# Kernel tuning notes

Hardware: AMD Instinct MI355X
Metric: run time of the kernel (lower is better)

Reference implementation:

```python
import jax, jax.numpy as jnp
import numpy as np

NVAR, B, C, H, W = 3, 4, 256, 64, 64
C1 = C // 2          # dat channels (nc)
C2 = C - C1
HEADS = 4
HC = C1 // HEADS     # head channels
STRIDE = 4
KS = 4
HK, WK = H // STRIDE, W // STRIDE
NS = HK * WK         # n_sample
RPE_H, RPE_W = 2 * H - 1, 2 * W - 1
NPAIR = 3


def _grid_sample(img, grid):
    # img [B,C,Hi,Wi]; grid [B,Hg,Wg,2] = (x,y) in [-1,1]; bilinear, align_corners=True, zero-pad
    Bn, Cn, Hi, Wi = img.shape
    x = (grid[..., 0] + 1.0) * 0.5 * (Wi - 1)
    y = (grid[..., 1] + 1.0) * 0.5 * (Hi - 1)
    x0 = jnp.floor(x)
    y0 = jnp.floor(y)
    wx = x - x0
    wy = y - y0
    x0i = x0.astype(jnp.int32)
    y0i = y0.astype(jnp.int32)
    imt = img.transpose(0, 2, 3, 1)  # [B,Hi,Wi,C]
    bidx = jnp.arange(Bn)[:, None, None]

    def corner(yi, xi, wgt):
        ok = ((xi >= 0) & (xi < Wi) & (yi >= 0) & (yi < Hi)).astype(img.dtype)
        val = imt[bidx, jnp.clip(yi, 0, Hi - 1), jnp.clip(xi, 0, Wi - 1)]  # [B,Hg,Wg,C]
        return val * (wgt * ok)[..., None]

    out = (corner(y0i, x0i, (1 - wx) * (1 - wy))
           + corner(y0i, x0i + 1, wx * (1 - wy))
           + corner(y0i + 1, x0i, (1 - wx) * wy)
           + corner(y0i + 1, x0i + 1, wx * wy))
    return out.transpose(0, 3, 1, 2)  # [B,C,Hg,Wg]


def _ref_points(hk, wk):
    # normalized sampling-grid reference points, (y,x) order
    ry = (jnp.linspace(0.5, hk - 0.5, hk) / (hk - 1.0)) * 2.0 - 1.0
    rx = (jnp.linspace(0.5, wk - 0.5, wk) / (wk - 1.0)) * 2.0 - 1.0
    return jnp.stack(jnp.meshgrid(ry, rx, indexing='ij'), axis=-1)  # [hk,wk,2]


def _q_grid(h, w):
    gy = (jnp.arange(h, dtype=jnp.float32) / (h - 1.0)) * 2.0 - 1.0
    gx = (jnp.arange(w, dtype=jnp.float32) / (w - 1.0)) * 2.0 - 1.0
    return jnp.stack(jnp.meshgrid(gy, gx, indexing='ij'), axis=-1).reshape(h * w, 2)


def _conv1x1(x, w, b=None):
    y = jnp.einsum('oc,bchw->bohw', w, x)
    return y if b is None else y + b[None, :, None, None]


def _dat_block(q_in, kv_in, pWq, pbq, pWk, pbk, pWv, pbv, pWo, pbo,
               pdw_w, pdw_b, pln_g, pln_b, ppw_w, prpe):
    Bn = q_in.shape[0]
    q = _conv1x1(q_in, pWq, pbq)  # [B,C1,H,W]
    # offset net: depthwise 4x4 stride-4 conv -> channel LN -> GELU -> 1x1 conv to 2
    off = jax.lax.conv_general_dilated(
        q, pdw_w, (STRIDE, STRIDE), 'VALID',
        dimension_numbers=('NCHW', 'OIHW', 'NCHW'),
        feature_group_count=C1) + pdw_b[None, :, None, None]  # [B,C1,HK,WK]
    mu = off.mean(axis=1, keepdims=True)
    var = ((off - mu) ** 2).mean(axis=1, keepdims=True)
    off = (off - mu) * jax.lax.rsqrt(var + 1e-5) * pln_g[None, :, None, None] + pln_b[None, :, None, None]
    off = jax.nn.gelu(off, approximate=False)
    offset = _conv1x1(off, ppw_w).transpose(0, 2, 3, 1)  # [B,HK,WK,2] (dy,dx)
    # offset_range_factor = -1 -> no tanh scaling, clamp pos into [-1,1]
    pos = jnp.clip(offset + _ref_points(HK, WK)[None], -1.0, 1.0)  # [B,HK,WK,2]
    xs = _grid_sample(kv_in, pos[..., ::-1])  # sample kv at deformed points -> [B,C1,HK,WK]
    k = _conv1x1(xs, pWk, pbk).reshape(Bn, HEADS, HC, NS)
    v = _conv1x1(xs, pWv, pbv).reshape(Bn, HEADS, HC, NS)
    qh = q.reshape(Bn, HEADS, HC, H * W)
    attn = jnp.einsum('bhcm,bhcn->bhmn', qh, k) * (HC ** -0.5)  # [B,h,HW,NS]
    # relative position bias sampled from rpe table
    disp = (_q_grid(H, W)[None, :, None, :] - pos.reshape(Bn, 1, NS, 2)) * 0.5  # [B,HW,NS,2]
    rpe_b = jnp.broadcast_to(prpe[None], (Bn, HEADS, RPE_H, RPE_W))
    bias = _grid_sample(rpe_b, disp[..., ::-1])  # [B,h,HW,NS]
    attn = jax.nn.softmax(attn + bias, axis=-1)
    out = jnp.einsum('bhmn,bhcn->bhcm', attn, v).reshape(Bn, C1, H, W)
    return _conv1x1(out, pWo, pbo)


def _forward(xs, params):
    results = []
    num = 0
    for i in range(NVAR):
        res = xs[i]
        for j in range(i):
            attn_out = _dat_block(xs[i][:, :C1], xs[j][:, :C1],
                                  *(p[num] for p in params))
            # torch: res -= -cat(zeros[:,:C2], attn)  => add attn on channels C2:
            res = res.at[:, C2:].add(attn_out)
            num += 1
        results.append(res)
    return jnp.stack(results)  # [NVAR,B,C,H,W]


def setup_inputs() -> dict:
    key = jax.random.key(0)
    ks = jax.random.split(key, 4)
    d = {}
    for n, k in zip(['x0', 'x1', 'x2'], jax.random.split(ks[0], 3)):
        d[n] = jax.random.normal(k, (B, C, H, W), jnp.float32)

    def w(k, shape, s=0.02):
        return jax.random.normal(k, shape, jnp.float32) * s

    kk = jax.random.split(ks[1], 8)
    d['Wq'] = w(kk[0], (NPAIR, C1, C1))
    d['bq'] = jnp.zeros((NPAIR, C1), jnp.float32)
    d['Wk'] = w(kk[1], (NPAIR, C1, C1))
    d['bk'] = jnp.zeros((NPAIR, C1), jnp.float32)
    d['Wv'] = w(kk[2], (NPAIR, C1, C1))
    d['bv'] = jnp.zeros((NPAIR, C1), jnp.float32)
    d['Wo'] = w(kk[3], (NPAIR, C1, C1))
    d['bo'] = jnp.zeros((NPAIR, C1), jnp.float32)
    d['dw_w'] = w(kk[4], (NPAIR, C1, 1, KS, KS), 0.1)
    d['dw_b'] = jnp.zeros((NPAIR, C1), jnp.float32)
    d['ln_g'] = jnp.ones((NPAIR, C1), jnp.float32)
    d['ln_b'] = jnp.zeros((NPAIR, C1), jnp.float32)
    d['pw_w'] = w(kk[5], (NPAIR, 2, C1), 0.1)
    d['rpe'] = w(kk[6], (NPAIR, HEADS, RPE_H, RPE_W), 0.01)
    return d


def reference(x0, x1, x2, Wq, bq, Wk, bk, Wv, bv, Wo, bo,
              dw_w, dw_b, ln_g, ln_b, pw_w, rpe):
    params = (Wq, bq, Wk, bk, Wv, bv, Wo, bo, dw_w, dw_b, ln_g, ln_b, pw_w, rpe)
    out = _forward([x0, x1, x2], params)
    flow = jnp.zeros((NVAR, x0.shape[0]), out.dtype)
    return out, flow
```

## Files before the change

kernel.cpp:

```cpp
#include <hip/hip_runtime.h>
#include <math.h>

#define NVAR 3
#define BB 4
#define CC 256
#define C1 128
#define HEADS 4
#define HH 64
#define WW 64
#define HW 4096
#define RPE_W 127
#define NP 3
#define SCALE 0.17677669529663687f

typedef short bf16x8 __attribute__((ext_vector_type(8)));
typedef float f32x4 __attribute__((ext_vector_type(4)));

__device__ __forceinline__ unsigned short f2bf(float f) {
    unsigned int u = __float_as_uint(f);
    u += 0x7fffu + ((u >> 16) & 1u);
    return (unsigned short)(u >> 16);
}
__device__ __forceinline__ float bflo(unsigned u) { return __uint_as_float(u << 16); }
__device__ __forceinline__ float bfhi(unsigned u) { return __uint_as_float(u & 0xffff0000u); }

__global__ __launch_bounds__(256) void copy_init(const float* __restrict__ x0,
                                                 float* __restrict__ out) {
    const long long n4 = (long long)BB * CC * HW / 4;
    long long stride = (long long)gridDim.x * blockDim.x;
    for (long long i = (long long)blockIdx.x * blockDim.x + threadIdx.x;
         i < n4 + 12; i += stride) {
        if (i < n4) ((float4*)out)[i] = ((const float4*)x0)[i];
        else out[3LL * BB * CC * HW + (i - n4)] = 0.f;
    }
}

__global__ __launch_bounds__(256) void prep_const(const float* __restrict__ rpe,
                                                  const float* __restrict__ Wq,
                                                  const float* __restrict__ Wo,
                                                  const float* __restrict__ Wk,
                                                  const float* __restrict__ Wv,
                                                  unsigned short* __restrict__ tabbf,
                                                  unsigned short* __restrict__ wqh,
                                                  unsigned short* __restrict__ wql,
                                                  unsigned short* __restrict__ woh,
                                                  unsigned short* __restrict__ wkh,
                                                  unsigned short* __restrict__ wvh) {
    int blk = blockIdx.x;
    if (blk < 12) {
        const float* src = rpe + (long long)blk * RPE_W * RPE_W;
        unsigned short* dst = tabbf + (long long)blk * 16384;
        for (int idx = threadIdx.x; idx < 16384; idx += 256) {
            int y = idx >> 7, x = idx & 127;
            float v = (y < RPE_W && x < RPE_W) ? src[y * RPE_W + x] : 0.f;
            dst[idx] = f2bf(v);
        }
    } else if (blk < 15) {
        int p = blk - 12;
        for (int i = threadIdx.x; i < 16384; i += 256) {
            float w = Wq[p * 16384 + i];
            unsigned short h = f2bf(w);
            wqh[p * 16384 + i] = h;
            wql[p * 16384 + i] = f2bf(w - bflo((unsigned)h));
        }
    } else if (blk < 18) {
        int p = blk - 15;
        for (int i = threadIdx.x; i < 16384; i += 256)
            woh[p * 16384 + i] = f2bf(Wo[p * 16384 + i]);
    } else if (blk < 21) {
        int p = blk - 18;
        for (int i = threadIdx.x; i < 16384; i += 256)
            wkh[p * 16384 + i] = f2bf(Wk[p * 16384 + i]);
    } else {
        int p = blk - 21;
        for (int i = threadIdx.x; i < 16384; i += 256)
            wvh[p * 16384 + i] = f2bf(Wv[p * 16384 + i]);
    }
}

__global__ __launch_bounds__(256) void conv_q(const float* __restrict__ x1,
                                              const float* __restrict__ x2,
                                              const unsigned short* __restrict__ wqh,
                                              const unsigned short* __restrict__ wql,
                                              const float* __restrict__ bq,
                                              float* __restrict__ qbuf,
                                              unsigned short* __restrict__ qbf,
                                              float* __restrict__ out) {
    int wid = threadIdx.x >> 6, lane = threadIdx.x & 63;
    int g = lane >> 4, lm = lane & 15;
    int gw = blockIdx.x * 4 + wid;
    int mt = gw & 255;
    int pb = gw >> 8;
    int p = pb >> 2, b = pb & 3;
    const float* X = ((p == 0) ? x1 : x2) + (long long)b * CC * HW;
    int m = mt * 16 + lm;
    float* outc = (p < 2)
        ? out + (((long long)((p + 1) * 4 + b)) * CC) * HW + m
        : nullptr;

    bf16x8 bhi[4], blo[4];
#pragma unroll
    for (int ksl = 0; ksl < 4; ksl++) {
        float v[8];
#pragma unroll
        for (int j = 0; j < 8; j++) {
            int k = ksl * 32 + 8 * g + j;
            v[j] = X[(long long)k * HW + m];
            if (outc) outc[(long long)k * HW] = v[j];
        }
        union { unsigned u[4]; bf16x8 v; } H, L;
#pragma unroll
        for (int t = 0; t < 4; t++) {
            unsigned short h0 = f2bf(v[2 * t]), h1 = f2bf(v[2 * t + 1]);
            unsigned short l0 = f2bf(v[2 * t] - bflo((unsigned)h0));
            unsigned short l1 = f2bf(v[2 * t + 1] - bflo((unsigned)h1));
            H.u[t] = (unsigned)h0 | ((unsigned)h1 << 16);
            L.u[t] = (unsigned)l0 | ((unsigned)l1 << 16);
        }
        bhi[ksl] = H.v;
        blo[ksl] = L.v;
    }

    const unsigned short* WH = wqh + p * 16384;
    const unsigned short* WL = wql + p * 16384;
    f32x4 zero = {0.f, 0.f, 0.f, 0.f};
#pragma unroll
    for (int ct2 = 0; ct2 < 4; ct2++) {
        int ct0 = 2 * ct2, ct1 = ct0 + 1;
        f32x4 a0 = zero, a1 = zero;
#pragma unroll
        for (int ksl = 0; ksl < 4; ksl++) {
            bf16x8 Ah0 = *(const bf16x8*)(WH + (ct0 * 16 + lm) * 128 + ksl * 32 + 8 * g);
            bf16x8 Al0 = *(const bf16x8*)(WL + (ct0 * 16 + lm) * 128 + ksl * 32 + 8 * g);
            bf16x8 Ah1 = *(const bf16x8*)(WH + (ct1 * 16 + lm) * 128 + ksl * 32 + 8 * g);
            bf16x8 Al1 = *(const bf16x8*)(WL + (ct1 * 16 + lm) * 128 + ksl * 32 + 8 * g);
            a0 = __builtin_amdgcn_mfma_f32_16x16x32_bf16(Ah0, bhi[ksl], a0, 0, 0, 0);
            a1 = __builtin_amdgcn_mfma_f32_16x16x32_bf16(Ah1, bhi[ksl], a1, 0, 0, 0);
            a0 = __builtin_amdgcn_mfma_f32_16x16x32_bf16(Ah0, blo[ksl], a0, 0, 0, 0);
            a1 = __builtin_amdgcn_mfma_f32_16x16x32_bf16(Ah1, blo[ksl], a1, 0, 0, 0);
            a0 = __builtin_amdgcn_mfma_f32_16x16x32_bf16(Al0, bhi[ksl], a0, 0, 0, 0);
            a1 = __builtin_amdgcn_mfma_f32_16x16x32_bf16(Al1, bhi[ksl], a1, 0, 0, 0);
        }
        float q0[4], q1[4];
#pragma unroll
        for (int r = 0; r < 4; r++) {
            int c0 = ct0 * 16 + 4 * g + r, c1 = ct1 * 16 + 4 * g + r;
            q0[r] = a0[r] + bq[p * 128 + c0];
            q1[r] = a1[r] + bq[p * 128 + c1];
            qbuf[((long long)pb * 128 + c0) * HW + m] = q0[r];
            qbuf[((long long)pb * 128 + c1) * HW + m] = q1[r];
        }
        unsigned short* Yb = qbf + ((long long)pb * HW + m) * 128;
        *(unsigned*)(Yb + ct0 * 16 + 4 * g) =
            (unsigned)f2bf(q0[0] * SCALE) | ((unsigned)f2bf(q0[1] * SCALE) << 16);
        *(unsigned*)(Yb + ct0 * 16 + 4 * g + 2) =
            (unsigned)f2bf(q0[2] * SCALE) | ((unsigned)f2bf(q0[3] * SCALE) << 16);
        *(unsigned*)(Yb + ct1 * 16 + 4 * g) =
            (unsigned)f2bf(q1[0] * SCALE) | ((unsigned)f2bf(q1[1] * SCALE) << 16);
        *(unsigned*)(Yb + ct1 * 16 + 4 * g + 2) =
            (unsigned)f2bf(q1[2] * SCALE) | ((unsigned)f2bf(q1[3] * SCALE) << 16);
    }
}

__global__ __launch_bounds__(256) void offset_dw(const float* __restrict__ qbuf,
                                                 const float* __restrict__ dw_w,
                                                 const float* __restrict__ dw_b,
                                                 float* __restrict__ off) {
    __shared__ float ld[32][4][65];
    int blk = blockIdx.x;
    int pb = blk >> 4;
    int hk = blk & 15;
    int p = pb >> 2;
    int tid = threadIdx.x;
    for (int cq = 0; cq < 4; cq++) {
        int c32 = cq * 32;
        __syncthreads();
#pragma unroll
        for (int it = 0; it < 8; it++) {
            int i2 = tid + it * 256;
            int c = i2 >> 6, rem = i2 & 63;
            int y = rem >> 4, xq = rem & 15;
            float4 v = *(const float4*)(qbuf + ((long long)pb * 128 + c32 + c) * HW
                                        + (4 * hk + y) * 64 + xq * 4);
            ld[c][y][xq * 4 + 0] = v.x;
            ld[c][y][xq * 4 + 1] = v.y;
            ld[c][y][xq * 4 + 2] = v.z;
            ld[c][y][xq * 4 + 3] = v.w;
        }
        __syncthreads();
        int wk = tid >> 4;
#pragma unroll
        for (int oi = 0; oi < 2; oi++) {
            int c = (tid & 15) + oi * 16;
            const float* dwp = dw_w + (p * 128 + c32 + c) * 16;
            float acc = dw_b[p * 128 + c32 + c];
#pragma unroll
            for (int ky = 0; ky < 4; ky++)
#pragma unroll
                for (int kx = 0; kx < 4; kx++)
                    acc += ld[c][ky][wk * 4 + kx] * dwp[ky * 4 + kx];
            off[((long long)pb * 256 + hk * 16 + wk) * 128 + c32 + c] = acc;
        }
    }
}

__global__ __launch_bounds__(64) void offset_ln(const float* __restrict__ off,
                                                const float* __restrict__ ln_g,
                                                const float* __restrict__ ln_b,
                                                const float* __restrict__ pw_w,
                                                float* __restrict__ posb,
                                                uint4* __restrict__ prmb) {
    int blk = blockIdx.x;
    int pb = blk >> 8;
    int s = blk & 255;
    int p = pb >> 2;
    int hk = s >> 4, wk = s & 15;
    int lane = threadIdx.x;
    const float* op = off + ((long long)pb * 256 + s) * 128;
    float a0 = op[lane], a1 = op[lane + 64];
    float s1 = a0 + a1;
#pragma unroll
    for (int o = 1; o < 64; o <<= 1) s1 += __shfl_xor(s1, o);
    float mu = s1 * (1.f / 128.f);
    float d0 = a0 - mu, d1 = a1 - mu;
    float v2 = d0 * d0 + d1 * d1;
#pragma unroll
    for (int o = 1; o < 64; o <<= 1) v2 += __shfl_xor(v2, o);
    float rs = rsqrtf(v2 * (1.f / 128.f) + 1e-5f);
    int c0 = lane, c1 = lane + 64;
    float y0 = d0 * rs * ln_g[p * 128 + c0] + ln_b[p * 128 + c0];
    float y1 = d1 * rs * ln_g[p * 128 + c1] + ln_b[p * 128 + c1];
    float g0 = 0.5f * y0 * (1.f + erff(y0 * 0.70710678118654752f));
    float g1 = 0.5f * y1 * (1.f + erff(y1 * 0.70710678118654752f));
    float o0 = pw_w[(p * 2 + 0) * 128 + c0] * g0 + pw_w[(p * 2 + 0) * 128 + c1] * g1;
    float o1 = pw_w[(p * 2 + 1) * 128 + c0] * g0 + pw_w[(p * 2 + 1) * 128 + c1] * g1;
#pragma unroll
    for (int o = 1; o < 64; o <<= 1) o0 += __shfl_xor(o0, o);
#pragma unroll
    for (int o = 1; o < 64; o <<= 1) o1 += __shfl_xor(o1, o);
    if (lane == 0) {
        float refy = (hk + 0.5f) * (2.f / 15.f) - 1.f;
        float refx = (wk + 0.5f) * (2.f / 15.f) - 1.f;
        float py = fminf(fmaxf(o0 + refy, -1.f), 1.f);
        float px = fminf(fmaxf(o1 + refx, -1.f), 1.f);
        int pbn = pb * 256 + s;
        posb[pbn * 2 + 0] = py;
        posb[pbn * 2 + 1] = px;
        float cy = 31.5f * (1.f - py), cx = 31.5f * (1.f - px);
        float yf = floorf(cy), xf = floorf(cx);
        float wy = cy - yf, wx = cx - xf;
        int Y0 = (int)yf, X0 = (int)xf;
        uint4 v;
        v.x = (unsigned)f2bf((1.f - wy) * (1.f - wx))
            | ((unsigned)f2bf((1.f - wy) * wx) << 16);
        v.y = (unsigned)f2bf(wy * (1.f - wx))
            | ((unsigned)f2bf(wy * wx) << 16);
        v.z = (unsigned)((Y0 * 128 + X0) * 2);
        v.w = 0;
        prmb[pbn] = v;
    }
}

__global__ __launch_bounds__(256) void trans_x(const float* __restrict__ x0,
                                               const float* __restrict__ x1,
                                               unsigned short* __restrict__ xT) {
    __shared__ float ld[32][65];
    int blk = blockIdx.x;
    int v = blk >> 10;
    int rem = blk & 1023;
    int b = rem >> 8;
    int rem2 = rem & 255;
    int ct = rem2 >> 6;
    int mt = rem2 & 63;
    const float* src = ((v == 0) ? x0 : x1) + (long long)b * CC * HW
                       + (long long)(ct * 32) * HW + mt * 64;
    int tid = threadIdx.x;
#pragma unroll
    for (int it = 0; it < 2; it++) {
        int c = tid >> 3, x4 = (tid & 7) + it * 8;
        float4 w = *(const float4*)(src + (long long)c * HW + x4 * 4);
        ld[c][x4 * 4 + 0] = w.x;
        ld[c][x4 * 4 + 1] = w.y;
        ld[c][x4 * 4 + 2] = w.z;
        ld[c][x4 * 4 + 3] = w.w;
    }
    __syncthreads();
    int m = tid >> 2, cg = tid & 3;
    union { unsigned u[4]; } pk;
#pragma unroll
    for (int t = 0; t < 4; t++) {
        unsigned short h0 = f2bf(ld[cg * 8 + 2 * t][m]);
        unsigned short h1 = f2bf(ld[cg * 8 + 2 * t + 1][m]);
        pk.u[t] = (unsigned)h0 | ((unsigned)h1 << 16);
    }
    *(uint4*)(xT + (((long long)(v * 4 + b)) * HW + mt * 64 + m) * 128
              + ct * 32 + cg * 8) = *(uint4*)pk.u;
}

__global__ __launch_bounds__(256) void sample_kv(const unsigned short* __restrict__ xT,
                                                 const float* __restrict__ posb,
                                                 const unsigned short* __restrict__ wkh,
                                                 const unsigned short* __restrict__ wvh,
                                                 const float* __restrict__ bk,
                                                 const float* __restrict__ bv,
                                                 unsigned short* __restrict__ kbf,
                                                 unsigned short* __restrict__ vbf) {
    __shared__ unsigned short xls[32 * 128];
    int blk = blockIdx.x;
    int pb = blk >> 3;
    int nt = blk & 7;
    int p = pb >> 2, b = pb & 3;
    int n0 = nt * 32;
    int tid = threadIdx.x;

    {
        int nl = tid >> 3, co = tid & 7;
        int n = n0 + nl;
        float py = posb[(pb * 256 + n) * 2 + 0];
        float px = posb[(pb * 256 + n) * 2 + 1];
        float yi = (py + 1.f) * 31.5f, xi = (px + 1.f) * 31.5f;
        yi = fminf(fmaxf(yi, 0.f), 63.f);
        xi = fminf(fmaxf(xi, 0.f), 63.f);
        int y0 = min((int)yi, 62);
        int x0i = min((int)xi, 62);
        float wy = yi - (float)y0, wx = xi - (float)x0i;
        float w00 = (1.f - wy) * (1.f - wx), w01 = (1.f - wy) * wx;
        float w10 = wy * (1.f - wx), w11 = wy * wx;
        int vsel = (p == 2) ? 1 : 0;
        const unsigned short* base = xT + ((long long)(vsel * 4 + b)) * HW * 128;
        int m00 = y0 * 64 + x0i;
        char* dst = (char*)xls;
#pragma unroll
        for (int cb = 0; cb < 2; cb++) {
            int c0 = co * 16 + cb * 8;
            bf16x8 a = *(const bf16x8*)(base + (long long)m00 * 128 + c0);
            bf16x8 bb = *(const bf16x8*)(base + (long long)(m00 + 1) * 128 + c0);
            bf16x8 cc = *(const bf16x8*)(base + (long long)(m00 + 64) * 128 + c0);
            bf16x8 dd = *(const bf16x8*)(base + (long long)(m00 + 65) * 128 + c0);
            union { unsigned u[4]; bf16x8 v; } R;
#pragma unroll
            for (int t = 0; t < 4; t++) {
                float r0 = w00 * bflo((unsigned)(unsigned short)a[2 * t])
                         + w01 * bflo((unsigned)(unsigned short)bb[2 * t])
                         + w10 * bflo((unsigned)(unsigned short)cc[2 * t])
                         + w11 * bflo((unsigned)(unsigned short)dd[2 * t]);
                float r1 = w00 * bflo((unsigned)(unsigned short)a[2 * t + 1])
                         + w01 * bflo((unsigned)(unsigned short)bb[2 * t + 1])
                         + w10 * bflo((unsigned)(unsigned short)cc[2 * t + 1])
                         + w11 * bflo((unsigned)(unsigned short)dd[2 * t + 1]);
                R.u[t] = (unsigned)f2bf(r0) | ((unsigned)f2bf(r1) << 16);
            }
            *(bf16x8*)(dst + ((nl * 256 + c0 * 2) ^ ((nl & 7) << 4))) = R.v;
        }
    }
    __syncthreads();

    int wid = tid >> 6, lane = tid & 63;
    int g = lane >> 4, lm = lane & 15;
    int ntile = wid & 1, isv = wid >> 1;
    int nl = ntile * 16 + lm;
    const char* srcl = (const char*)xls;
    bf16x8 xf[4];
#pragma unroll
    for (int ks = 0; ks < 4; ks++)
        xf[ks] = *(const bf16x8*)(srcl + ((nl * 256 + (ks * 32 + 8 * g) * 2)
                                          ^ ((nl & 7) << 4)));
    f32x4 zero = {0.f, 0.f, 0.f, 0.f};
    if (!isv) {
        const unsigned short* WK = wkh + p * 16384;
#pragma unroll
        for (int ct = 0; ct < 8; ct++) {
            f32x4 acc = zero;
#pragma unroll
            for (int ks = 0; ks < 4; ks++) {
                bf16x8 wf = *(const bf16x8*)(WK + (ct * 16 + lm) * 128 + ks * 32 + 8 * g);
                acc = __builtin_amdgcn_mfma_f32_16x16x32_bf16(xf[ks], wf, acc, 0, 0, 0);
            }
            float bias = bk[p * 128 + ct * 16 + lm];
#pragma unroll
            for (int r = 0; r < 4; r++) {
                int n = n0 + ntile * 16 + 4 * g + r;
                kbf[((long long)pb * 256 + n) * 128 + ct * 16 + lm] = f2bf(acc[r] + bias);
            }
        }
    } else {
        const unsigned short* WV = wvh + p * 16384;
#pragma unroll
        for (int ct = 0; ct < 8; ct++) {
            f32x4 acc = zero;
#pragma unroll
            for (int ks = 0; ks < 4; ks++) {
                bf16x8 wf = *(const bf16x8*)(WV + (ct * 16 + lm) * 128 + ks * 32 + 8 * g);
                acc = __builtin_amdgcn_mfma_f32_16x16x32_bf16(wf, xf[ks], acc, 0, 0, 0);
            }
#pragma unroll
            for (int r = 0; r < 4; r++) {
                int c = ct * 16 + 4 * g + r;
                vbf[((long long)pb * 128 + c) * 256 + n0 + ntile * 16 + lm]
                    = f2bf(acc[r] + bv[p * 128 + c]);
            }
        }
    }
}

__global__ __launch_bounds__(256, 4) void attn_mfma(
        const unsigned short* __restrict__ qbf,
        const unsigned short* __restrict__ kbf,
        const unsigned short* __restrict__ vbf,
        const unsigned short* __restrict__ tabbf,
        const uint4* __restrict__ prmb,
        float* __restrict__ obuf) {
    __shared__ unsigned short tab[16384];
    __shared__ uint4 prm[256];
    int tid = threadIdx.x;
    int wid = tid >> 6, lane = tid & 63;
    int g = lane >> 4, lm = lane & 15;
    int bid = blockIdx.x;
    int my = bid & 63;
    int h = (bid >> 6) & 3;
    int b = (bid >> 8) & 3;
    int p = bid >> 10;
    int pb = p * 4 + b;

    {
        const uint4* ts = (const uint4*)(tabbf + (long long)(p * 4 + h) * 16384);
        uint4* td = (uint4*)tab;
#pragma unroll
        for (int i = 0; i < 8; i++) td[tid + i * 256] = ts[tid + i * 256];
        prm[tid] = prmb[pb * 256 + tid];
    }
    __syncthreads();

    int mx = (wid << 4) + lm;

    bf16x8 qf = *(const bf16x8*)(qbf + ((long long)pb * HW + my * 64 + mx) * 128
                                 + h * 32 + 8 * g);
    const unsigned short* kbase = kbf + ((long long)pb * 256 + lm) * 128
                                  + h * 32 + 8 * g;
    f32x4 zero = {0.f, 0.f, 0.f, 0.f};
    f32x4 acc[16];
#pragma unroll
    for (int ni = 0; ni < 16; ni++) {
        bf16x8 kf = *(const bf16x8*)(kbase + ni * 16 * 128);
        acc[ni] = __builtin_amdgcn_mfma_f32_16x16x32_bf16(kf, qf, zero, 0, 0, 0);
    }

    int laneoff = (my * 128 + mx) * 2;
    const char* tb = (const char*)tab;
#pragma unroll
    for (int ni = 0; ni < 16; ni++) {
#pragma unroll
        for (int r = 0; r < 4; r++) {
            int n = ni * 16 + 4 * g + r;
            uint4 pw = prm[n];
            int va = (int)pw.z + laneoff;
            float a0 = bflo(*(const unsigned short*)(tb + va));
            float a1 = bflo(*(const unsigned short*)(tb + va + 2));
            float b0 = bflo(*(const unsigned short*)(tb + va + 256));
            float b1 = bflo(*(const unsigned short*)(tb + va + 258));
            float t = fmaf(bflo(pw.x), a0, acc[ni][r]);
            t = fmaf(bfhi(pw.x), a1, t);
            t = fmaf(bflo(pw.y), b0, t);
            t = fmaf(bfhi(pw.y), b1, t);
            acc[ni][r] = t;
        }
    }

    float mxv = -1e30f;
#pragma unroll
    for (int ni = 0; ni < 16; ni++)
        mxv = fmaxf(mxv, fmaxf(fmaxf(acc[ni][0], acc[ni][1]),
                               fmaxf(acc[ni][2], acc[ni][3])));
    mxv = fmaxf(mxv, __shfl_xor(mxv, 16));
    mxv = fmaxf(mxv, __shfl_xor(mxv, 32));
    float sum = 0.f;
    unsigned dwA[16], dwB[16];
#pragma unroll
    for (int ni = 0; ni < 16; ni++) {
        float e0 = __expf(acc[ni][0] - mxv);
        float e1 = __expf(acc[ni][1] - mxv);
        float e2 = __expf(acc[ni][2] - mxv);
        float e3 = __expf(acc[ni][3] - mxv);
        sum += (e0 + e1) + (e2 + e3);
        asm("v_cvt_pk_bf16_f32 %0, %1, %2" : "=v"(dwA[ni]) : "v"(e0), "v"(e1));
        asm("v_cvt_pk_bf16_f32 %0, %1, %2" : "=v"(dwB[ni]) : "v"(e2), "v"(e3));
    }
    sum += __shfl_xor(sum, 16);
    sum += __shfl_xor(sum, 32);

    int src0 = ((g & 1) << 5) + lm;
    int src1 = src0 + 16;
    bool sel = (g >> 1) != 0;
    const unsigned short* vb0 = vbf + ((long long)pb * 128 + h * 32 + lm) * 256
                                + 8 * g;
    f32x4 o0 = zero, o1 = zero;
#pragma unroll
    for (int st = 0; st < 8; st++) {
        unsigned d0a = __shfl(dwA[2 * st], src0), d0b = __shfl(dwA[2 * st + 1], src0);
        unsigned d1a = __shfl(dwB[2 * st], src0), d1b = __shfl(dwB[2 * st + 1], src0);
        unsigned d2a = __shfl(dwA[2 * st], src1), d2b = __shfl(dwA[2 * st + 1], src1);
        unsigned d3a = __shfl(dwB[2 * st], src1), d3b = __shfl(dwB[2 * st + 1], src1);
        union { unsigned u[4]; bf16x8 v; } pf;
        pf.u[0] = sel ? d0b : d0a;
        pf.u[1] = sel ? d1b : d1a;
        pf.u[2] = sel ? d2b : d2a;
        pf.u[3] = sel ? d3b : d3a;
        bf16x8 v0 = *(const bf16x8*)(vb0 + st * 32);
        bf16x8 v1 = *(const bf16x8*)(vb0 + 4096 + st * 32);
        o0 = __builtin_amdgcn_mfma_f32_16x16x32_bf16(v0, pf.v, o0, 0, 0, 0);
        o1 = __builtin_amdgcn_mfma_f32_16x16x32_bf16(v1, pf.v, o1, 0, 0, 0);
    }

    float inv = 1.f / sum;
    float* ob = obuf + ((long long)pb * 128 + h * 32) * HW + my * 64 + mx;
#pragma unroll
    for (int r = 0; r < 4; r++) {
        ob[(g * 4 + r) * HW] = o0[r] * inv;
        ob[(16 + g * 4 + r) * HW] = o1[r] * inv;
    }
}

__global__ __launch_bounds__(256) void conv_wo(const float* __restrict__ x1,
                                               const float* __restrict__ x2,
                                               const float* __restrict__ obuf,
                                               const unsigned short* __restrict__ woh,
                                               const float* __restrict__ bo,
                                               float* __restrict__ out) {
    int wid = threadIdx.x >> 6, lane = threadIdx.x & 63;
    int g = lane >> 4, lm = lane & 15;
    int gw = blockIdx.x * 4 + wid;
    int mt = gw & 255;
    int b = (gw >> 8) & 3;
    int vs = gw >> 10;
    int m = mt * 16 + lm;
    int np = vs + 1;

    f32x4 acc[8];
#pragma unroll
    for (int ct = 0; ct < 8; ct++) acc[ct] = (f32x4){0.f, 0.f, 0.f, 0.f};

    for (int pi = 0; pi < np; pi++) {
        int p = vs ? (1 + pi) : 0;
        const float* O = obuf + (long long)(p * 4 + b) * 128 * HW;
        bf16x8 bh[4];
#pragma unroll
        for (int ksl = 0; ksl < 4; ksl++) {
            float v[8];
#pragma unroll
            for (int j = 0; j < 8; j++)
                v[j] = O[(long long)(ksl * 32 + 8 * g + j) * HW + m];
            union { unsigned u[4]; bf16x8 v; } H;
#pragma unroll
            for (int t = 0; t < 4; t++)
                H.u[t] = (unsigned)f2bf(v[2 * t]) | ((unsigned)f2bf(v[2 * t + 1]) << 16);
            bh[ksl] = H.v;
        }
        const unsigned short* WH = woh + p * 16384;
#pragma unroll
        for (int ct = 0; ct < 8; ct++)
#pragma unroll
            for (int ksl = 0; ksl < 4; ksl++) {
                bf16x8 A = *(const bf16x8*)(WH + (ct * 16 + lm) * 128 + ksl * 32 + 8 * g);
                acc[ct] = __builtin_amdgcn_mfma_f32_16x16x32_bf16(A, bh[ksl], acc[ct], 0, 0, 0);
            }
    }

    int qi = vs + 1;
    const float* xq = (vs ? x2 : x1) + (long long)b * CC * HW;
#pragma unroll
    for (int ct = 0; ct < 8; ct++)
#pragma unroll
        for (int r = 0; r < 4; r++) {
            int c = ct * 16 + 4 * g + r;
            float bias = vs ? (bo[128 + c] + bo[256 + c]) : bo[c];
            float base = xq[(long long)(128 + c) * HW + m];
            out[(((long long)(qi * 4 + b)) * CC + 128 + c) * HW + m]
                = base + acc[ct][r] + bias;
        }
}

extern "C" void kernel_launch(void* const* d_in, const int* in_sizes, int n_in,
                              void* d_out, int out_size, void* d_ws, size_t ws_size,
                              hipStream_t stream) {
    const float* x0 = (const float*)d_in[0];
    const float* x1 = (const float*)d_in[1];
    const float* x2 = (const float*)d_in[2];
    const float* Wq = (const float*)d_in[3];
    const float* bq = (const float*)d_in[4];
    const float* Wk = (const float*)d_in[5];
    const float* bk = (const float*)d_in[6];
    const float* Wv = (const float*)d_in[7];
    const float* bv = (const float*)d_in[8];
    const float* Wo = (const float*)d_in[9];
    const float* bo = (const float*)d_in[10];
    const float* dw_w = (const float*)d_in[11];
    const float* dw_b = (const float*)d_in[12];
    const float* ln_g = (const float*)d_in[13];
    const float* ln_b = (const float*)d_in[14];
    const float* pw_w = (const float*)d_in[15];
    const float* rpe = (const float*)d_in[16];
    float* out = (float*)d_out;

    float* ws = (float*)d_ws;
    float* qbuf = ws;
    unsigned short* xT = (unsigned short*)ws;
    float* obuf = ws;
    float* posb = ws + 6291456;
    float* off  = posb + 6144;
    unsigned short* qbf = (unsigned short*)(off + 393216);
    unsigned short* kbf = qbf + 12582912;
    unsigned short* vbf = kbf + 393216;
    unsigned short* tabbf = vbf + 393216;
    uint4* prmb = (uint4*)(tabbf + 196608);
    unsigned short* wqh = (unsigned short*)(prmb + 3072);
    unsigned short* wql = wqh + 49152;
    unsigned short* woh = wql + 49152;
    unsigned short* wkh = woh + 49152;
    unsigned short* wvh = wkh + 49152;

    copy_init<<<1024, 256, 0, stream>>>(x0, out);
    prep_const<<<24, 256, 0, stream>>>(rpe, Wq, Wo, Wk, Wv, tabbf,
                                       wqh, wql, woh, wkh, wvh);
    conv_q<<<768, 256, 0, stream>>>(x1, x2, wqh, wql, bq, qbuf, qbf, out);
    offset_dw<<<192, 256, 0, stream>>>(qbuf, dw_w, dw_b, off);
    offset_ln<<<3072, 64, 0, stream>>>(off, ln_g, ln_b, pw_w, posb, prmb);
    trans_x<<<2048, 256, 0, stream>>>(x0, x1, xT);
    sample_kv<<<96, 256, 0, stream>>>(xT, posb, wkh, wvh, bk, bv, kbf, vbf);
    attn_mfma<<<3072, 256, 0, stream>>>(qbf, kbf, vbf, tabbf, prmb, obuf);
    conv_wo<<<512, 256, 0, stream>>>(x1, x2, obuf, woh, bo, out);
}
```

Before: 188.6 us.

## Merge small kernels, use dot2 bf16 for RPE bilinear, add MFMA priority hints

Folds copy_init into prep_const, and folds offset_dw, offset_ln and trans_x into one mid_kernel that keeps the depthwise-conv output in shared memory instead of a global off buffer. This cuts kernel launches and a global round trip. In attention, the four scalar bf16 table reads per sample become two aligned 32-bit reads combined with alignbyte and fdot2 bf16. s_setprio is placed around the MFMA sections. xT gets its own workspace region because the transpose now runs concurrently with the phase that reads qbuf. fdot2 rounding may differ slightly from separate fmas.

New measurement: 181.6 us. 3.7% less time.

```diff
diff --git a/kernel.cpp b/kernel.cpp
--- a/kernel.cpp
+++ b/kernel.cpp
@@ -15,6 +15,7 @@
 
 typedef short bf16x8 __attribute__((ext_vector_type(8)));
 typedef float f32x4 __attribute__((ext_vector_type(4)));
+typedef __bf16 bf16x2 __attribute__((ext_vector_type(2)));
 
 __device__ __forceinline__ unsigned short f2bf(float f) {
     unsigned int u = __float_as_uint(f);
@@ -24,29 +25,39 @@
 __device__ __forceinline__ float bflo(unsigned u) { return __uint_as_float(u << 16); }
 __device__ __forceinline__ float bfhi(unsigned u) { return __uint_as_float(u & 0xffff0000u); }
 
-__global__ __launch_bounds__(256) void copy_init(const float* __restrict__ x0,
+__device__ __forceinline__ float dot2bf(unsigned a, unsigned b, float c) {
+#if __has_builtin(__builtin_amdgcn_fdot2_f32_bf16)
+    return __builtin_amdgcn_fdot2_f32_bf16(__builtin_bit_cast(bf16x2, a),
+                                           __builtin_bit_cast(bf16x2, b), c, false);
+#else
+    return c + bflo(a) * bflo(b) + bfhi(a) * bfhi(b);
+#endif
+}
+
+__global__ __launch_bounds__(256) void prep_copy(const float* __restrict__ rpe,
+                                                 const float* __restrict__ Wq,
+                                                 const float* __restrict__ Wo,
+                                                 const float* __restrict__ Wk,
+                                                 const float* __restrict__ Wv,
+                                                 const float* __restrict__ x0,
+                                                 unsigned short* __restrict__ tabbf,
+                                                 unsigned short* __restrict__ wqh,
+                                                 unsigned short* __restrict__ wql,
+                                                 unsigned short* __restrict__ woh,
+                                                 unsigned short* __restrict__ wkh,
+                                                 unsigned short* __restrict__ wvh,
                                                  float* __restrict__ out) {
-    const long long n4 = (long long)BB * CC * HW / 4;
-    long long stride = (long long)gridDim.x * blockDim.x;
-    for (long long i = (long long)blockIdx.x * blockDim.x + threadIdx.x;
-         i < n4 + 12; i += stride) {
-        if (i < n4) ((float4*)out)[i] = ((const float4*)x0)[i];
-        else out[3LL * BB * CC * HW + (i - n4)] = 0.f;
-    }
-}
-
-__global__ __launch_bounds__(256) void prep_const(const float* __restrict__ rpe,
-                                                  const float* __restrict__ Wq,
-                                                  const float* __restrict__ Wo,
-                                                  const float* __restrict__ Wk,
-                                                  const float* __restrict__ Wv,
-                                                  unsigned short* __restrict__ tabbf,
-                                                  unsigned short* __restrict__ wqh,
-                                                  unsigned short* __restrict__ wql,
-                                                  unsigned short* __restrict__ woh,
-                                                  unsigned short* __restrict__ wkh,
-                                                  unsigned short* __restrict__ wvh) {
     int blk = blockIdx.x;
+    if (blk >= 24) {
+        const long long n4 = (long long)BB * CC * HW / 4;
+        long long i = (long long)(blk - 24) * 256 + threadIdx.x;
+        const long long stride = 1024LL * 256;
+        for (; i < n4 + 12; i += stride) {
+            if (i < n4) ((float4*)out)[i] = ((const float4*)x0)[i];
+            else out[3LL * BB * CC * HW + (i - n4)] = 0.f;
+        }
+        return;
+    }
     if (blk < 12) {
         const float* src = rpe + (long long)blk * RPE_W * RPE_W;
         unsigned short* dst = tabbf + (long long)blk * 16384;
@@ -162,139 +173,138 @@
     }
 }
 
-__global__ __launch_bounds__(256) void offset_dw(const float* __restrict__ qbuf,
-                                                 const float* __restrict__ dw_w,
-                                                 const float* __restrict__ dw_b,
-                                                 float* __restrict__ off) {
-    __shared__ float ld[32][4][65];
+__global__ __launch_bounds__(256) void mid_kernel(const float* __restrict__ qbuf,
+                                                  const float* __restrict__ dw_w,
+                                                  const float* __restrict__ dw_b,
+                                                  const float* __restrict__ ln_g,
+                                                  const float* __restrict__ ln_b,
+                                                  const float* __restrict__ pw_w,
+                                                  const float* __restrict__ x0,
+                                                  const float* __restrict__ x1,
+                                                  float* __restrict__ posb,
+                                                  uint4* __restrict__ prmb,
+                                                  unsigned short* __restrict__ xT) {
+    __shared__ float sm[32 * 4 * 65 + 16 * 128];
     int blk = blockIdx.x;
-    int pb = blk >> 4;
-    int hk = blk & 15;
-    int p = pb >> 2;
     int tid = threadIdx.x;
-    for (int cq = 0; cq < 4; cq++) {
-        int c32 = cq * 32;
+    if (blk < 192) {
+        float (*ld)[4][65] = (float(*)[4][65])sm;
+        float (*dwout)[128] = (float(*)[128])(sm + 32 * 4 * 65);
+        int pb = blk >> 4, hk = blk & 15;
+        int p = pb >> 2;
+        for (int cq = 0; cq < 4; cq++) {
+            int c32 = cq * 32;
+            __syncthreads();
+#pragma unroll
+            for (int it = 0; it < 8; it++) {
+                int i2 = tid + it * 256;
+                int c = i2 >> 6, rem = i2 & 63;
+                int y = rem >> 4, xq = rem & 15;
+                float4 v = *(const float4*)(qbuf + ((long long)pb * 128 + c32 + c) * HW
+                                            + (4 * hk + y) * 64 + xq * 4);
+                ld[c][y][xq * 4 + 0] = v.x;
+                ld[c][y][xq * 4 + 1] = v.y;
+                ld[c][y][xq * 4 + 2] = v.z;
+                ld[c][y][xq * 4 + 3] = v.w;
+            }
+            __syncthreads();
+            int wk = tid >> 4;
+#pragma unroll
+            for (int oi = 0; oi < 2; oi++) {
+                int c = (tid & 15) + oi * 16;
+                const float* dwp = dw_w + (p * 128 + c32 + c) * 16;
+                float acc = dw_b[p * 128 + c32 + c];
+#pragma unroll
+                for (int ky = 0; ky < 4; ky++)
+#pragma unroll
+                    for (int kx = 0; kx < 4; kx++)
+                        acc += ld[c][ky][wk * 4 + kx] * dwp[ky * 4 + kx];
+                dwout[wk][c32 + c] = acc;
+            }
+        }
         __syncthreads();
-#pragma unroll
-        for (int it = 0; it < 8; it++) {
-            int i2 = tid + it * 256;
-            int c = i2 >> 6, rem = i2 & 63;
-            int y = rem >> 4, xq = rem & 15;
-            float4 v = *(const float4*)(qbuf + ((long long)pb * 128 + c32 + c) * HW
-                                        + (4 * hk + y) * 64 + xq * 4);
-            ld[c][y][xq * 4 + 0] = v.x;
-            ld[c][y][xq * 4 + 1] = v.y;
-            ld[c][y][xq * 4 + 2] = v.z;
-            ld[c][y][xq * 4 + 3] = v.w;
+        int wid = tid >> 6, lane = tid & 63;
+        for (int i = 0; i < 4; i++) {
+            int wk = wid * 4 + i;
+            int s = hk * 16 + wk;
+            float a0 = dwout[wk][lane], a1 = dwout[wk][lane + 64];
+            float s1 = a0 + a1;
+#pragma unroll
+            for (int o = 1; o < 64; o <<= 1) s1 += __shfl_xor(s1, o);
+            float mu = s1 * (1.f / 128.f);
+            float d0 = a0 - mu, d1 = a1 - mu;
+            float v2 = d0 * d0 + d1 * d1;
+#pragma unroll
+            for (int o = 1; o < 64; o <<= 1) v2 += __shfl_xor(v2, o);
+            float rs = rsqrtf(v2 * (1.f / 128.f) + 1e-5f);
+            int c0 = lane, c1 = lane + 64;
+            float y0 = d0 * rs * ln_g[p * 128 + c0] + ln_b[p * 128 + c0];
+            float y1 = d1 * rs * ln_g[p * 128 + c1] + ln_b[p * 128 + c1];
+            float g0 = 0.5f * y0 * (1.f + erff(y0 * 0.70710678118654752f));
+            float g1 = 0.5f * y1 * (1.f + erff(y1 * 0.70710678118654752f));
+            float o0 = pw_w[(p * 2 + 0) * 128 + c0] * g0
+                     + pw_w[(p * 2 + 0) * 128 + c1] * g1;
+            float o1 = pw_w[(p * 2 + 1) * 128 + c0] * g0
+                     + pw_w[(p * 2 + 1) * 128 + c1] * g1;
+#pragma unroll
+            for (int o = 1; o < 64; o <<= 1) o0 += __shfl_xor(o0, o);
+#pragma unroll
+            for (int o = 1; o < 64; o <<= 1) o1 += __shfl_xor(o1, o);
+            if (lane == 0) {
+                int wk2 = s & 15;
+                float refy = (hk + 0.5f) * (2.f / 15.f) - 1.f;
+                float refx = (wk2 + 0.5f) * (2.f / 15.f) - 1.f;
+                float py = fminf(fmaxf(o0 + refy, -1.f), 1.f);
+                float px = fminf(fmaxf(o1 + refx, -1.f), 1.f);
+                int pbn = pb * 256 + s;
+                posb[pbn * 2 + 0] = py;
+                posb[pbn * 2 + 1] = px;
+                float cy = 31.5f * (1.f - py), cx = 31.5f * (1.f - px);
+                float yf = floorf(cy), xf = floorf(cx);
+                float wy = cy - yf, wx = cx - xf;
+                int Y0 = (int)yf, X0 = (int)xf;
+                uint4 v;
+                v.x = (unsigned)f2bf((1.f - wy) * (1.f - wx))
+                    | ((unsigned)f2bf((1.f - wy) * wx) << 16);
+                v.y = (unsigned)f2bf(wy * (1.f - wx))
+                    | ((unsigned)f2bf(wy * wx) << 16);
+                v.z = (unsigned)((Y0 * 128 + X0) * 2);
+                v.w = 0;
+                prmb[pbn] = v;
+            }
+        }
+    } else {
+        float (*ld2)[65] = (float(*)[65])sm;
+        int rem = blk - 192;
+        int v = rem >> 10;
+        int rem1 = rem & 1023;
+        int b = rem1 >> 8;
+        int rem2 = rem1 & 255;
+        int ct = rem2 >> 6;
+        int mt = rem2 & 63;
+        const float* src = ((v == 0) ? x0 : x1) + (long long)b * CC * HW
+                           + (long long)(ct * 32) * HW + mt * 64;
+#pragma unroll
+        for (int it = 0; it < 2; it++) {
+            int c = tid >> 3, x4 = (tid & 7) + it * 8;
+            float4 w = *(const float4*)(src + (long long)c * HW + x4 * 4);
+            ld2[c][x4 * 4 + 0] = w.x;
+            ld2[c][x4 * 4 + 1] = w.y;
+            ld2[c][x4 * 4 + 2] = w.z;
+            ld2[c][x4 * 4 + 3] = w.w;
         }
         __syncthreads();
-        int wk = tid >> 4;
-#pragma unroll
-        for (int oi = 0; oi < 2; oi++) {
-            int c = (tid & 15) + oi * 16;
-            const float* dwp = dw_w + (p * 128 + c32 + c) * 16;
-            float acc = dw_b[p * 128 + c32 + c];
-#pragma unroll
-            for (int ky = 0; ky < 4; ky++)
-#pragma unroll
-                for (int kx = 0; kx < 4; kx++)
-                    acc += ld[c][ky][wk * 4 + kx] * dwp[ky * 4 + kx];
-            off[((long long)pb * 256 + hk * 16 + wk) * 128 + c32 + c] = acc;
-        }
-    }
-}
-
-__global__ __launch_bounds__(64) void offset_ln(const float* __restrict__ off,
-                                                const float* __restrict__ ln_g,
-                                                const float* __restrict__ ln_b,
-                                                const float* __restrict__ pw_w,
-                                                float* __restrict__ posb,
-                                                uint4* __restrict__ prmb) {
-    int blk = blockIdx.x;
-    int pb = blk >> 8;
-    int s = blk & 255;
-    int p = pb >> 2;
-    int hk = s >> 4, wk = s & 15;
-    int lane = threadIdx.x;
-    const float* op = off + ((long long)pb * 256 + s) * 128;
-    float a0 = op[lane], a1 = op[lane + 64];
-    float s1 = a0 + a1;
-#pragma unroll
-    for (int o = 1; o < 64; o <<= 1) s1 += __shfl_xor(s1, o);
-    float mu = s1 * (1.f / 128.f);
-    float d0 = a0 - mu, d1 = a1 - mu;
-    float v2 = d0 * d0 + d1 * d1;
-#pragma unroll
-    for (int o = 1; o < 64; o <<= 1) v2 += __shfl_xor(v2, o);
-    float rs = rsqrtf(v2 * (1.f / 128.f) + 1e-5f);
-    int c0 = lane, c1 = lane + 64;
-    float y0 = d0 * rs * ln_g[p * 128 + c0] + ln_b[p * 128 + c0];
-    float y1 = d1 * rs * ln_g[p * 128 + c1] + ln_b[p * 128 + c1];
-    float g0 = 0.5f * y0 * (1.f + erff(y0 * 0.70710678118654752f));
-    float g1 = 0.5f * y1 * (1.f + erff(y1 * 0.70710678118654752f));
-    float o0 = pw_w[(p * 2 + 0) * 128 + c0] * g0 + pw_w[(p * 2 + 0) * 128 + c1] * g1;
-    float o1 = pw_w[(p * 2 + 1) * 128 + c0] * g0 + pw_w[(p * 2 + 1) * 128 + c1] * g1;
-#pragma unroll
-    for (int o = 1; o < 64; o <<= 1) o0 += __shfl_xor(o0, o);
-#pragma unroll
-    for (int o = 1; o < 64; o <<= 1) o1 += __shfl_xor(o1, o);
-    if (lane == 0) {
-        float refy = (hk + 0.5f) * (2.f / 15.f) - 1.f;
-        float refx = (wk + 0.5f) * (2.f / 15.f) - 1.f;
-        float py = fminf(fmaxf(o0 + refy, -1.f), 1.f);
-        float px = fminf(fmaxf(o1 + refx, -1.f), 1.f);
-        int pbn = pb * 256 + s;
-        posb[pbn * 2 + 0] = py;
-        posb[pbn * 2 + 1] = px;
-        float cy = 31.5f * (1.f - py), cx = 31.5f * (1.f - px);
-        float yf = floorf(cy), xf = floorf(cx);
-        float wy = cy - yf, wx = cx - xf;
-        int Y0 = (int)yf, X0 = (int)xf;
-        uint4 v;
-        v.x = (unsigned)f2bf((1.f - wy) * (1.f - wx))
-            | ((unsigned)f2bf((1.f - wy) * wx) << 16);
-        v.y = (unsigned)f2bf(wy * (1.f - wx))
-            | ((unsigned)f2bf(wy * wx) << 16);
-        v.z = (unsigned)((Y0 * 128 + X0) * 2);
-        v.w = 0;
-        prmb[pbn] = v;
-    }
-}
-
-__global__ __launch_bounds__(256) void trans_x(const float* __restrict__ x0,
-                                               const float* __restrict__ x1,
-                                               unsigned short* __restrict__ xT) {
-    __shared__ float ld[32][65];
-    int blk = blockIdx.x;
-    int v = blk >> 10;
-    int rem = blk & 1023;
-    int b = rem >> 8;
-    int rem2 = rem & 255;
-    int ct = rem2 >> 6;
-    int mt = rem2 & 63;
-    const float* src = ((v == 0) ? x0 : x1) + (long long)b * CC * HW
-                       + (long long)(ct * 32) * HW + mt * 64;
-    int tid = threadIdx.x;
-#pragma unroll
-    for (int it = 0; it < 2; it++) {
-        int c = tid >> 3, x4 = (tid & 7) + it * 8;
-        float4 w = *(const float4*)(src + (long long)c * HW + x4 * 4);
-        ld[c][x4 * 4 + 0] = w.x;
-        ld[c][x4 * 4 + 1] = w.y;
-        ld[c][x4 * 4 + 2] = w.z;
-        ld[c][x4 * 4 + 3] = w.w;
-    }
-    __syncthreads();
-    int m = tid >> 2, cg = tid & 3;
-    union { unsigned u[4]; } pk;
-#pragma unroll
-    for (int t = 0; t < 4; t++) {
-        unsigned short h0 = f2bf(ld[cg * 8 + 2 * t][m]);
-        unsigned short h1 = f2bf(ld[cg * 8 + 2 * t + 1][m]);
-        pk.u[t] = (unsigned)h0 | ((unsigned)h1 << 16);
-    }
-    *(uint4*)(xT + (((long long)(v * 4 + b)) * HW + mt * 64 + m) * 128
-              + ct * 32 + cg * 8) = *(uint4*)pk.u;
+        int m = tid >> 2, cg = tid & 3;
+        union { unsigned u[4]; } pk;
+#pragma unroll
+        for (int t = 0; t < 4; t++) {
+            unsigned short h0 = f2bf(ld2[cg * 8 + 2 * t][m]);
+            unsigned short h1 = f2bf(ld2[cg * 8 + 2 * t + 1][m]);
+            pk.u[t] = (unsigned)h0 | ((unsigned)h1 << 16);
+        }
+        *(uint4*)(xT + (((long long)(v * 4 + b)) * HW + mt * 64 + m) * 128
+                  + ct * 32 + cg * 8) = *(uint4*)pk.u;
+    }
 }
 
 __global__ __launch_bounds__(256) void sample_kv(const unsigned short* __restrict__ xT,
@@ -410,7 +420,7 @@
         const unsigned short* __restrict__ tabbf,
         const uint4* __restrict__ prmb,
         float* __restrict__ obuf) {
-    __shared__ unsigned short tab[16384];
+    __shared__ unsigned short tab[16384 + 8];
     __shared__ uint4 prm[256];
     int tid = threadIdx.x;
     int wid = tid >> 6, lane = tid & 63;
@@ -439,11 +449,13 @@
                                   + h * 32 + 8 * g;
     f32x4 zero = {0.f, 0.f, 0.f, 0.f};
     f32x4 acc[16];
+    __builtin_amdgcn_s_setprio(1);
 #pragma unroll
     for (int ni = 0; ni < 16; ni++) {
         bf16x8 kf = *(const bf16x8*)(kbase + ni * 16 * 128);
         acc[ni] = __builtin_amdgcn_mfma_f32_16x16x32_bf16(kf, qf, zero, 0, 0, 0);
     }
+    __builtin_amdgcn_s_setprio(0);
 
     int laneoff = (my * 128 + mx) * 2;
     const char* tb = (const char*)tab;
@@ -454,14 +466,17 @@
             int n = ni * 16 + 4 * g + r;
             uint4 pw = prm[n];
             int va = (int)pw.z + laneoff;
-            float a0 = bflo(*(const unsigned short*)(tb + va));
-            float a1 = bflo(*(const unsigned short*)(tb + va + 2));
-            float b0 = bflo(*(const unsigned short*)(tb + va + 256));
-            float b1 = bflo(*(const unsigned short*)(tb + va + 258));
-            float t = fmaf(bflo(pw.x), a0, acc[ni][r]);
-            t = fmaf(bfhi(pw.x), a1, t);
-            t = fmaf(bflo(pw.y), b0, t);
-            t = fmaf(bfhi(pw.y), b1, t);
+            int va4 = va & ~3;
+            int sh = va & 3;
+            unsigned r0 = *(const unsigned*)(tb + va4);
+            unsigned r1 = *(const unsigned*)(tb + va4 + 4);
+            unsigned r2 = *(const unsigned*)(tb + va4 + 256);
+            unsigned r3 = *(const unsigned*)(tb + va4 + 260);
+            unsigned p0 = __builtin_amdgcn_alignbyte(r1, r0, sh);
+            unsigned p1 = __builtin_amdgcn_alignbyte(r3, r2, sh);
+            float t = acc[ni][r];
+            t = dot2bf(p0, pw.x, t);
+            t = dot2bf(p1, pw.y, t);
             acc[ni][r] = t;
         }
     }
@@ -507,8 +522,10 @@
         pf.u[3] = sel ? d3b : d3a;
         bf16x8 v0 = *(const bf16x8*)(vb0 + st * 32);
         bf16x8 v1 = *(const bf16x8*)(vb0 + 4096 + st * 32);
+        __builtin_amdgcn_s_setprio(1);
         o0 = __builtin_amdgcn_mfma_f32_16x16x32_bf16(v0, pf.v, o0, 0, 0, 0);
         o1 = __builtin_amdgcn_mfma_f32_16x16x32_bf16(v1, pf.v, o1, 0, 0, 0);
+        __builtin_amdgcn_s_setprio(0);
     }
 
     float inv = 1.f / sum;
@@ -603,11 +620,10 @@
 
     float* ws = (float*)d_ws;
     float* qbuf = ws;
-    unsigned short* xT = (unsigned short*)ws;
-    float* obuf = ws;
+    float* obuf = qbuf;
     float* posb = ws + 6291456;
-    float* off  = posb + 6144;
-    unsigned short* qbf = (unsigned short*)(off + 393216);
+    unsigned short* xT = (unsigned short*)(posb + 6144);
+    unsigned short* qbf = xT + 4194304;
     unsigned short* kbf = qbf + 12582912;
     unsigned short* vbf = kbf + 393216;
     unsigned short* tabbf = vbf + 393216;
@@ -618,13 +634,11 @@
     unsigned short* wkh = woh + 49152;
     unsigned short* wvh = wkh + 49152;
 
-    copy_init<<<1024, 256, 0, stream>>>(x0, out);
-    prep_const<<<24, 256, 0, stream>>>(rpe, Wq, Wo, Wk, Wv, tabbf,
-                                       wqh, wql, woh, wkh, wvh);
+    prep_copy<<<1048, 256, 0, stream>>>(rpe, Wq, Wo, Wk, Wv, x0, tabbf,
+                                        wqh, wql, woh, wkh, wvh, out);
     conv_q<<<768, 256, 0, stream>>>(x1, x2, wqh, wql, bq, qbuf, qbf, out);
-    offset_dw<<<192, 256, 0, stream>>>(qbuf, dw_w, dw_b, off);
-    offset_ln<<<3072, 64, 0, stream>>>(off, ln_g, ln_b, pw_w, posb, prmb);
-    trans_x<<<2048, 256, 0, stream>>>(x0, x1, xT);
+    mid_kernel<<<2240, 256, 0, stream>>>(qbuf, dw_w, dw_b, ln_g, ln_b, pw_w,
+                                         x0, x1, posb, prmb, xT);
     sample_kv<<<96, 256, 0, stream>>>(xT, posb, wkh, wvh, bk, bv, kbf, vbf);
     attn_mfma<<<3072, 256, 0, stream>>>(qbf, kbf, vbf, tabbf, prmb, obuf);
     conv_wo<<<512, 256, 0, stream>>>(x1, x2, obuf, woh, bo, out);
```
